# Optimization experiments

Hardware: AMD Instinct MI355X
Metric: run time of the kernel (lower is better)

The kernel has to match this reference:

```python
import jax, jax.numpy as jnp
import numpy as np

N = 100000      # entity nodes
E = 1000000     # edges per relation
D_IN = 256
HID = 128
EPS = 1e-16     # PyG softmax denominator eps
NEG_SLOPE = 0.2 # GATConv default leaky_relu slope


def _gat_conv(x, ei, Ws, Wd, a_s, a_d, b):
    """Single-head GATConv (heads=1, concat=False) with self-loops."""
    n = x.shape[0]
    loop = jnp.arange(n, dtype=ei.dtype)
    src = jnp.concatenate([ei[0], loop])  # [E+N]
    dst = jnp.concatenate([ei[1], loop])
    h_src = x @ Ws                         # [N, HID]
    h_dst = x @ Wd                         # [N, HID]
    a_src = h_src @ a_s                    # [N]
    a_dst = h_dst @ a_d                    # [N]
    e = jax.nn.leaky_relu(a_src[src] + a_dst[dst], NEG_SLOPE)  # [E+N]
    # numerically-stable softmax over incoming edges of each dst node
    m = jax.ops.segment_max(e, dst, num_segments=n)
    ex = jnp.exp(e - m[dst])
    denom = jax.ops.segment_sum(ex, dst, num_segments=n)
    alpha = ex / (denom[dst] + EPS)        # [E+N]
    out = jax.ops.segment_sum(alpha[:, None] * h_src[src], dst, num_segments=n)
    return out + b


def setup_inputs() -> dict:
    key = jax.random.key(0)
    ks = jax.random.split(key, 9)
    s_in = 1.0 / np.sqrt(D_IN)
    s_h = 1.0 / np.sqrt(HID)
    return {
        "x": jax.random.normal(ks[0], (N, D_IN), dtype=jnp.float32),
        "edge_index_r0": jax.random.randint(ks[1], (2, E), 0, N, dtype=jnp.int64)
                         if jax.config.jax_enable_x64 else jax.random.randint(ks[1], (2, E), 0, N).astype(jnp.int32),
        "edge_index_r1": jax.random.randint(ks[2], (2, E), 0, N, dtype=jnp.int64)
                         if jax.config.jax_enable_x64 else jax.random.randint(ks[2], (2, E), 0, N).astype(jnp.int32),
        "W_src": jax.random.normal(ks[3], (2, D_IN, HID), dtype=jnp.float32) * s_in,
        "W_dst": jax.random.normal(ks[4], (2, D_IN, HID), dtype=jnp.float32) * s_in,
        "att_src": jax.random.normal(ks[5], (2, HID), dtype=jnp.float32) * s_h,
        "att_dst": jax.random.normal(ks[6], (2, HID), dtype=jnp.float32) * s_h,
        "bias": jnp.zeros((2, HID), dtype=jnp.float32),
    }


def reference(x, edge_index_r0, edge_index_r1, W_src, W_dst, att_src, att_dst, bias):
    # HeteroConv aggr='sum' over the two entity->entity relations
    out = _gat_conv(x, edge_index_r0, W_src[0], W_dst[0], att_src[0], att_dst[0], bias[0])
    out = out + _gat_conv(x, edge_index_r1, W_src[1], W_dst[1], att_src[1], att_dst[1], bias[1])
    # ELU; dropout p=0.0 is identity
    return jax.nn.elu(out)
```

## Files before the change

kernel.cpp:

```cpp
#include <hip/hip_runtime.h>

typedef __attribute__((ext_vector_type(8))) __bf16 bf16x8;
typedef __attribute__((ext_vector_type(4))) float floatx4;
typedef __attribute__((ext_vector_type(2))) float floatx2;

__device__ __forceinline__ float bf2f(unsigned short u) {
    return __uint_as_float(((unsigned)u) << 16);
}
__device__ __forceinline__ unsigned short f2bf(float f) {
    unsigned u = __float_as_uint(f);
    unsigned r = u + 0x7FFFu + ((u >> 16) & 1u);
    return (unsigned short)(r >> 16);
}

__device__ __forceinline__ void canon8(const void* src, unsigned short* dst,
                                       long long idx, int f) {
    if (f) {
        *(uint4*)&dst[idx] = *(const uint4*)((const unsigned short*)src + idx);
    } else {
        const float* sf = (const float*)src;
        unsigned short v[8];
        for (int j = 0; j < 8; ++j) v[j] = f2bf(sf[idx + j]);
        *(uint4*)&dst[idx] = *(const uint4*)v;
    }
}

__global__ void detect_k(const unsigned short* __restrict__ xs, int* __restrict__ flag) {
    __shared__ int sred[256];
    int tid = threadIdx.x;
    int cnt = 0;
    for (int j = 0; j < 16; ++j) {
        unsigned short u = xs[(tid * 16 + j) * 2];
        int e = (u >> 7) & 0xFF;
        cnt += (e >= 96 && e <= 159) ? 1 : 0;
    }
    sred[tid] = cnt;
    __syncthreads();
    for (int s = 128; s > 0; s >>= 1) {
        if (tid < s) sred[tid] += sred[tid + s];
        __syncthreads();
    }
    if (tid == 0) *flag = (sred[0] > 2048) ? 1 : 0;
}

__global__ void vecb_k(const void* __restrict__ Ws, const void* __restrict__ Wd,
                       const void* __restrict__ as, const void* __restrict__ ad,
                       const void* __restrict__ b, float* __restrict__ vecs,
                       unsigned short* __restrict__ bsb, const int* __restrict__ flag) {
    int blk = blockIdx.x, tid = threadIdx.x;
    int f = *flag;
    if (blk < 2) {
        int r = blk, k = tid;
        float s = 0.f, t = 0.f;
        if (f) {
            const unsigned short* wsrow = (const unsigned short*)Ws + (size_t)r * 32768 + (size_t)k * 128;
            const unsigned short* wdrow = (const unsigned short*)Wd + (size_t)r * 32768 + (size_t)k * 128;
            const unsigned short* asr = (const unsigned short*)as + r * 128;
            const unsigned short* adr = (const unsigned short*)ad + r * 128;
            for (int h = 0; h < 128; ++h) {
                s += bf2f(wsrow[h]) * bf2f(asr[h]);
                t += bf2f(wdrow[h]) * bf2f(adr[h]);
            }
        } else {
            const float* wsrow = (const float*)Ws + (size_t)r * 32768 + (size_t)k * 128;
            const float* wdrow = (const float*)Wd + (size_t)r * 32768 + (size_t)k * 128;
            const float* asr = (const float*)as + r * 128;
            const float* adr = (const float*)ad + r * 128;
            for (int h = 0; h < 128; ++h) {
                s += wsrow[h] * asr[h];
                t += wdrow[h] * adr[h];
            }
        }
        vecs[(r * 2 + 0) * 256 + k] = s;
        vecs[(r * 2 + 1) * 256 + k] = t;
    } else {
        if (tid < 32) canon8(b, bsb, (long long)tid * 8, f);
    }
}

__global__ __launch_bounds__(256) void mix1_k(
    const int* __restrict__ ei0, const int* __restrict__ ei1,
    int* __restrict__ cnt0, int* __restrict__ cnt1,
    int* __restrict__ rank0, int* __restrict__ rank1, int E_, int histB, int period,
    const void* __restrict__ xraw, unsigned short* __restrict__ xb,
    const float* __restrict__ vecs, float* __restrict__ aout, int n, int canB,
    unsigned long long* __restrict__ pair0, unsigned long long* __restrict__ pair1,
    int ps2, int zB,
    const void* __restrict__ Ws, unsigned short* __restrict__ Bt,
    const int* __restrict__ flag) {
    __shared__ float sv[1024];
    int b = blockIdx.x, tid = threadIdx.x;
    int bq = b / period;
    if (b - bq * period == 0) {
        if (bq >= histB) return;
        int rel = bq & 1;
        int t = ((bq >> 1) << 8) + tid;
        if (t >= E_ + n) return;
        const int* ei = rel ? ei1 : ei0;
        int* cnt = rel ? cnt1 : cnt0;
        int* rank = rel ? rank1 : rank0;
        int d = (t < E_) ? ei[E_ + t] : (t - E_);
        rank[t] = atomicAdd(&cnt[d], 1);
        return;
    }
    int oid = b - bq - 1;
    if (oid < canB) {
        for (int j = 0; j < 4; ++j) sv[j * 256 + tid] = vecs[j * 256 + tid];
        __syncthreads();
        int lane = tid & 63, wave = tid >> 6;
        int row = oid * 4 + wave;
        if (row >= n) return;
        float xf[4];
        if (*flag) {
            uint2 u = *(const uint2*)((const unsigned short*)xraw + (size_t)row * 256 + lane * 4);
            xf[0] = bf2f((unsigned short)(u.x & 0xFFFF));
            xf[1] = bf2f((unsigned short)(u.x >> 16));
            xf[2] = bf2f((unsigned short)(u.y & 0xFFFF));
            xf[3] = bf2f((unsigned short)(u.y >> 16));
        } else {
            float4 f = *(const float4*)((const float*)xraw + (size_t)row * 256 + lane * 4);
            xf[0] = f.x; xf[1] = f.y; xf[2] = f.z; xf[3] = f.w;
            unsigned short v[4] = {f2bf(f.x), f2bf(f.y), f2bf(f.z), f2bf(f.w)};
            *(uint2*)&xb[(size_t)row * 256 + lane * 4] = *(const uint2*)v;
        }
        float s[4] = {0.f, 0.f, 0.f, 0.f};
        for (int j = 0; j < 4; ++j)
            for (int q = 0; q < 4; ++q)
                s[j] += xf[q] * sv[j * 256 + lane * 4 + q];
        for (int j = 0; j < 4; ++j)
            for (int off = 32; off > 0; off >>= 1)
                s[j] += __shfl_down(s[j], off);
        if (lane == 0)
            for (int j = 0; j < 4; ++j) aout[(size_t)j * n + row] = s[j];
        return;
    }
    oid -= canB;
    if (oid < 2 * zB) {
        unsigned long long* dst = (oid < zB) ? pair0 : pair1;
        int z = (oid < zB) ? oid : oid - zB;
        int idx = z * 256 + tid;
        if (idx < ps2) ((uint4*)dst)[idx] = make_uint4(0u, 0u, 0u, 0u);
        return;
    }
    oid -= 2 * zB;
    if (oid < 256) {
        int i = oid * 256 + tid;
        int f = *flag;
        int r = i >> 15, rem = i & 32767;
        int k = rem >> 7, nn = rem & 127;
        unsigned short w = f ? ((const unsigned short*)Ws)[i]
                             : f2bf(((const float*)Ws)[i]);
        Bt[(size_t)r * 32768 + nn * 256 + k] = w;
    }
}

__global__ __launch_bounds__(256) void scan_red_k(const int* __restrict__ cnt0,
                                                  const int* __restrict__ cnt1,
                                                  int* __restrict__ part,
                                                  int n, int nb) {
    __shared__ int s[256];
    int rel = blockIdx.y;
    const int* cnt = rel ? cnt1 : cnt0;
    int i = blockIdx.x * 256 + threadIdx.x;
    int v = (i < n) ? ((cnt[i] + 7) & ~7) : 0;
    s[threadIdx.x] = v;
    __syncthreads();
    for (int o = 128; o > 0; o >>= 1) {
        if (threadIdx.x < o) s[threadIdx.x] += s[threadIdx.x + o];
        __syncthreads();
    }
    if (threadIdx.x == 0) part[rel * nb + blockIdx.x] = s[0];
}

__global__ __launch_bounds__(1024) void scan_mid_k(int* __restrict__ part, int nb) {
    __shared__ int s[1024];
    int rel = blockIdx.x;
    int t = threadIdx.x;
    s[t] = (t < nb) ? part[rel * nb + t] : 0;
    __syncthreads();
    for (int o = 1; o < 1024; o <<= 1) {
        int v = (t >= o) ? s[t - o] : 0;
        __syncthreads();
        s[t] += v;
        __syncthreads();
    }
    if (t < nb) part[rel * nb + t] = (t == 0) ? 0 : s[t - 1];
}

__global__ __launch_bounds__(256) void scan_off_k(const int* __restrict__ cnt0,
                                                  const int* __restrict__ cnt1,
                                                  const int* __restrict__ part,
                                                  int* __restrict__ off0,
                                                  int* __restrict__ off1,
                                                  int n, int nb) {
    __shared__ int s[256];
    int rel = blockIdx.y;
    const int* cnt = rel ? cnt1 : cnt0;
    int* off = rel ? off1 : off0;
    int i = blockIdx.x * 256 + threadIdx.x;
    int t = threadIdx.x;
    int v = (i < n) ? ((cnt[i] + 7) & ~7) : 0;
    s[t] = v;
    __syncthreads();
    for (int o = 1; o < 256; o <<= 1) {
        int u = (t >= o) ? s[t - o] : 0;
        __syncthreads();
        s[t] += u;
        __syncthreads();
    }
    if (i < n) off[i] = part[rel * nb + blockIdx.x] + s[t] - v;
}

__global__ void fill2_k(const int* __restrict__ ei0, const int* __restrict__ ei1,
                        const float* __restrict__ avals,
                        const int* __restrict__ off0, const int* __restrict__ off1,
                        const int* __restrict__ rank0, const int* __restrict__ rank1,
                        unsigned long long* __restrict__ pair0,
                        unsigned long long* __restrict__ pair1,
                        int E_, int n) {
    int rel = blockIdx.y;
    const int* ei = rel ? ei1 : ei0;
    const float* as_ = avals + (rel ? 2 * (size_t)n : 0);
    const float* ad_ = avals + (rel ? 3 * (size_t)n : (size_t)n);
    const int* off = rel ? off1 : off0;
    const int* rank = rel ? rank1 : rank0;
    unsigned long long* pair = rel ? pair1 : pair0;
    int t = blockIdx.x * 256 + threadIdx.x;
    if (t >= E_ + n) return;
    int s, d;
    if (t < E_) { s = ei[t]; d = ei[E_ + t]; } else { s = t - E_; d = s; }
    float e = as_[s] + ad_[d];
    e = e > 0.f ? e : 0.2f * e;
    float w = __expf(e);
    int pos = off[d] + rank[t];
    pair[pos] = ((unsigned long long)__float_as_uint(w) << 32) | (unsigned)s;
}

__device__ __forceinline__ void gload_lds16(const void* g, void* l) {
    __builtin_amdgcn_global_load_lds((const __attribute__((address_space(1))) void*)g,
                                     (__attribute__((address_space(3))) void*)l, 16, 0, 0);
}

__global__ __launch_bounds__(256) void gemm_h(const void* __restrict__ x_raw,
                                              const unsigned short* __restrict__ xb,
                                              const unsigned short* __restrict__ Btg,
                                              unsigned short* __restrict__ hout, int n,
                                              const int* __restrict__ flag) {
    const unsigned short* x = (*flag) ? (const unsigned short*)x_raw : xb;
    const int r = blockIdx.y;
    const unsigned short* bt = Btg + (size_t)r * 32768;
    unsigned short* h = hout + (size_t)r * n * 128;
    const int r0 = blockIdx.x * 128;
    __shared__ __align__(16) unsigned short As[128 * 64];
    __shared__ __align__(16) unsigned short Bs[128 * 64];
    int tid = threadIdx.x;
    int lane = tid & 63, wave = tid >> 6;
    int wm = wave >> 1, wn = wave & 1;

    floatx4 acc[4][4];
    for (int mt = 0; mt < 4; ++mt)
        for (int nt = 0; nt < 4; ++nt)
            acc[mt][nt] = (floatx4){0.f, 0.f, 0.f, 0.f};

    int srow = lane >> 3;
    int q    = lane & 7;
    int m16  = lane & 15;
    int qb   = lane >> 4;

    for (int k0 = 0; k0 < 256; k0 += 64) {
        for (int i = 0; i < 4; ++i) {
            int L = wave * 4 + i;
            int row = L * 8 + srow;
            int sw = ((q ^ (row & 7)) << 3);
            int grow = min(r0 + row, n - 1);
            gload_lds16(x + (size_t)grow * 256 + k0 + sw, &As[L * 512]);
            gload_lds16(bt + (size_t)row * 256 + k0 + sw, &Bs[L * 512]);
        }
        __syncthreads();
        for (int s = 0; s < 2; ++s) {
            int qr = qb + s * 4;
            bf16x8 af[4], bfv[4];
            for (int mt = 0; mt < 4; ++mt) {
                int row = wm * 64 + mt * 16 + m16;
                af[mt] = *(const bf16x8*)&As[row * 64 + ((qr ^ (row & 7)) << 3)];
            }
            for (int nt = 0; nt < 4; ++nt) {
                int row = wn * 64 + nt * 16 + m16;
                bfv[nt] = *(const bf16x8*)&Bs[row * 64 + ((qr ^ (row & 7)) << 3)];
            }
            for (int mt = 0; mt < 4; ++mt)
                for (int nt = 0; nt < 4; ++nt)
                    acc[mt][nt] = __builtin_amdgcn_mfma_f32_16x16x32_bf16(
                        af[mt], bfv[nt], acc[mt][nt], 0, 0, 0);
        }
        __syncthreads();
    }
    for (int mt = 0; mt < 4; ++mt) {
        int baser = r0 + wm * 64 + mt * 16 + qb * 4;
        for (int nt = 0; nt < 4; ++nt) {
            int c = wn * 64 + nt * 16 + m16;
            for (int i = 0; i < 4; ++i) {
                int gr = baser + i;
                if (gr < n) h[(size_t)gr * 128 + c] = f2bf(acc[mt][nt][i]);
            }
        }
    }
}

__device__ __forceinline__ void acc8pk(floatx2* a, float w, const uint4& hv) {
    floatx2 wv = {w, w};
    const unsigned u[4] = {hv.x, hv.y, hv.z, hv.w};
#pragma unroll
    for (int k = 0; k < 4; ++k) {
        floatx2 hf;
        hf.x = __uint_as_float(u[k] << 16);
        hf.y = __uint_as_float(u[k] & 0xFFFF0000u);
        asm("v_pk_fma_f32 %0, %1, %2, %0" : "+v"(a[k]) : "v"(wv), "v"(hf));
    }
}

__device__ __forceinline__ void rel_accP(int s0, int nIt, int g, unsigned l4,
                                         const unsigned long long* __restrict__ pair,
                                         const char* __restrict__ h8,
                                         floatx2* __restrict__ a, float& den) {
    int i = s0 + g;
    unsigned long long p0 = pair[i];
    unsigned long long p1 = pair[i + 4];
    for (int it = 0; it < nIt; ++it) {
        i += 8;
        unsigned long long q0 = pair[i];
        unsigned long long q1 = pair[i + 4];
        uint4 h0 = *(const uint4*)(h8 + ((((unsigned)p0) << 8) + l4));
        uint4 h1 = *(const uint4*)(h8 + ((((unsigned)p1) << 8) + l4));
        float w0 = __uint_as_float((unsigned)(p0 >> 32));
        float w1 = __uint_as_float((unsigned)(p1 >> 32));
        den += w0 + w1;
        acc8pk(a, w0, h0);
        acc8pk(a, w1, h1);
        p0 = q0; p1 = q1;
    }
}

__global__ __launch_bounds__(256) void agg_k(
    const int* __restrict__ off0, const int* __restrict__ cnt0,
    const unsigned long long* __restrict__ pair0,
    const int* __restrict__ off1, const int* __restrict__ cnt1,
    const unsigned long long* __restrict__ pair1,
    const char* __restrict__ h0, const char* __restrict__ h1,
    const unsigned short* __restrict__ bias, void* __restrict__ out,
    int n, const int* __restrict__ flag) {
    int wave = threadIdx.x >> 6, lane = threadIdx.x & 63;
    int g = lane >> 4, l = lane & 15;
    unsigned l4 = (unsigned)l << 4;
    int d = blockIdx.x * 4 + wave;
    if (d >= n) return;

    int sA = off0[d], nItA = (cnt0[d] + 7) >> 3;
    int sB = off1[d], nItB = (cnt1[d] + 7) >> 3;

    float denA = 0.f, denB = 0.f;
    floatx2 aA[4], aB[4];
#pragma unroll
    for (int k = 0; k < 4; ++k) {
        aA[k] = (floatx2){0.f, 0.f};
        aB[k] = (floatx2){0.f, 0.f};
    }
    rel_accP(sA, nItA, g, l4, pair0, h0, aA, denA);
    rel_accP(sB, nItB, g, l4, pair1, h1, aB, denB);

    denA += __shfl_xor(denA, 16);
    denA += __shfl_xor(denA, 32);
    denB += __shfl_xor(denB, 16);
    denB += __shfl_xor(denB, 32);
    float invA = __builtin_amdgcn_rcpf(denA + 1e-16f);
    float invB = __builtin_amdgcn_rcpf(denB + 1e-16f);
    floatx2 ivA = {invA, invA}, ivB = {invB, invB};
#pragma unroll
    for (int k = 0; k < 4; ++k) {
        asm("v_pk_mul_f32 %0, %0, %1" : "+v"(aA[k]) : "v"(ivA));
        asm("v_pk_fma_f32 %0, %1, %2, %0" : "+v"(aA[k]) : "v"(aB[k]), "v"(ivB));
    }
    float t8[8] = {aA[0].x, aA[0].y, aA[1].x, aA[1].y,
                   aA[2].x, aA[2].y, aA[3].x, aA[3].y};

    uint4 b0 = *(const uint4*)&bias[l * 8];
    uint4 b1 = *(const uint4*)&bias[128 + l * 8];
    const unsigned* b0u = (const unsigned*)&b0;
    const unsigned* b1u = (const unsigned*)&b1;
    float v[8];
#pragma unroll
    for (int j = 0; j < 8; ++j) {
        float s = t8[j];
        s += __shfl_xor(s, 16);
        s += __shfl_xor(s, 32);
        unsigned w0 = b0u[j >> 1], w1 = b1u[j >> 1];
        float bb = bf2f((unsigned short)((j & 1) ? (w0 >> 16) : (w0 & 0xFFFFu)))
                 + bf2f((unsigned short)((j & 1) ? (w1 >> 16) : (w1 & 0xFFFFu)));
        float t = s + bb;
        v[j] = t > 0.f ? t : (__expf(t) - 1.f);
    }
    if (g == 0) {
        if (*flag) {
            unsigned pk[4];
            for (int j = 0; j < 4; ++j)
                pk[j] = ((unsigned)f2bf(v[2 * j + 1]) << 16) | (unsigned)f2bf(v[2 * j]);
            ((uint4*)out)[(size_t)d * 16 + l] = *(const uint4*)pk;
        } else {
            float4 f0 = make_float4(v[0], v[1], v[2], v[3]);
            float4 f1 = make_float4(v[4], v[5], v[6], v[7]);
            ((float4*)out)[(size_t)d * 32 + l * 2] = f0;
            ((float4*)out)[(size_t)d * 32 + l * 2 + 1] = f1;
        }
    }
}

static inline char* carve(char*& p, size_t bytes) {
    char* r = p;
    p += (bytes + 255) & ~(size_t)255;
    return r;
}

extern "C" void kernel_launch(void* const* d_in, const int* in_sizes, int n_in,
                              void* d_out, int out_size, void* d_ws, size_t ws_size,
                              hipStream_t stream) {
    (void)n_in; (void)out_size; (void)ws_size;
    const void* x_raw  = d_in[0];
    const int*  ei0    = (const int*)d_in[1];
    const int*  ei1    = (const int*)d_in[2];
    const void* Ws_raw = d_in[3];
    const void* Wd_raw = d_in[4];
    const void* as_raw = d_in[5];
    const void* ad_raw = d_in[6];
    const void* b_raw  = d_in[7];

    const int n = in_sizes[0] / 256;
    const int e = in_sizes[1] / 2;
    const int tot = e + n;
    const int nb = (n + 255) / 256;
    const int PS = tot + 7 * n + 32;
    const int ps2 = PS / 2;
    const int zB = (ps2 + 255) / 256;

    char* p = (char*)d_ws;
    float* avals = (float*)carve(p, (size_t)4 * n * 4);
    int*   cnt0  = (int*)carve(p, (size_t)2 * n * 4);
    int*   cnt1  = cnt0 + n;
    int*   off0  = (int*)carve(p, (size_t)n * 4);
    int*   off1  = (int*)carve(p, (size_t)n * 4);
    int*   part  = (int*)carve(p, (size_t)2 * nb * 4);
    int*   rank0 = (int*)carve(p, (size_t)tot * 4);
    int*   rank1 = (int*)carve(p, (size_t)tot * 4);
    unsigned long long* pair0 = (unsigned long long*)carve(p, (size_t)PS * 8);
    unsigned long long* pair1 = (unsigned long long*)carve(p, (size_t)PS * 8);
    float* vecs  = (float*)carve(p, 1024 * 4);
    int*   flag  = (int*)carve(p, 256);
    unsigned short* xb  = (unsigned short*)carve(p, (size_t)(n + 128) * 256 * 2);
    unsigned short* h0  = (unsigned short*)carve(p, (size_t)2 * n * 128 * 2);
    unsigned short* h1  = h0 + (size_t)n * 128;
    unsigned short* Bt  = (unsigned short*)carve(p, 65536 * 2);
    unsigned short* bsb = (unsigned short*)carve(p, 256 * 2);

    hipMemsetAsync(cnt0, 0, (size_t)2 * n * 4, stream);

    detect_k<<<1, 256, 0, stream>>>((const unsigned short*)x_raw, flag);
    vecb_k<<<3, 256, 0, stream>>>(Ws_raw, Wd_raw, as_raw, ad_raw, b_raw,
                                  vecs, bsb, flag);

    int gb = (tot + 255) / 256;
    int histB = gb * 2;
    int canB = (n + 3) / 4;
    int otherTotal = canB + 2 * zB + 256;
    int period = (otherTotal + histB - 1) / histB + 1;
    int G = histB * period;
    mix1_k<<<G, 256, 0, stream>>>(
        ei0, ei1, cnt0, cnt1, rank0, rank1, e, histB, period,
        x_raw, xb, vecs, avals, n, canB,
        pair0, pair1, ps2, zB,
        Ws_raw, Bt, flag);

    scan_red_k<<<dim3(nb, 2), 256, 0, stream>>>(cnt0, cnt1, part, n, nb);
    scan_mid_k<<<2, 1024, 0, stream>>>(part, nb);
    scan_off_k<<<dim3(nb, 2), 256, 0, stream>>>(cnt0, cnt1, part, off0, off1, n, nb);

    fill2_k<<<dim3(gb, 2), 256, 0, stream>>>(ei0, ei1, avals, off0, off1,
                                             rank0, rank1, pair0, pair1, e, n);
    gemm_h<<<dim3((n + 127) / 128, 2), 256, 0, stream>>>(x_raw, xb, Bt, h0, n, flag);

    agg_k<<<(n + 3) / 4, 256, 0, stream>>>(off0, cnt0, pair0, off1, cnt1, pair1,
                                           (const char*)h0, (const char*)h1,
                                           bsb, d_out, n, flag);
}
```

Measured before the change: 436.6 us.

## Fuse GEMM into mixed histogram kernel and pad degree counters per cache line

Moves the bf16 MFMA GEMM that produces h into the multi-role mix1 kernel, so it runs alongside the atomic degree histogram, the attention-logit computation and the pair zeroing. In the fp32 path the input is converted to bf16 on the fly instead of first writing an xb copy. The weight transpose moves into the earlier prep kernel. Degree counters are spaced 64 bytes apart to reduce atomic contention on shared lines. In exchange, mix1 gets larger LDS usage and more registers, which may lower occupancy for its lightweight block roles, and the padded counters make the memset and the scan reads larger.

```diff
diff --git a/kernel.cpp b/kernel.cpp
--- a/kernel.cpp
+++ b/kernel.cpp
@@ -43,14 +43,22 @@
     if (tid == 0) *flag = (sred[0] > 2048) ? 1 : 0;
 }
 
-__global__ void vecb_k(const void* __restrict__ Ws, const void* __restrict__ Wd,
+__global__ void prep_k(const void* __restrict__ Ws, const void* __restrict__ Wd,
                        const void* __restrict__ as, const void* __restrict__ ad,
-                       const void* __restrict__ b, float* __restrict__ vecs,
+                       const void* __restrict__ b,
+                       unsigned short* __restrict__ Bt, float* __restrict__ vecs,
                        unsigned short* __restrict__ bsb, const int* __restrict__ flag) {
     int blk = blockIdx.x, tid = threadIdx.x;
     int f = *flag;
-    if (blk < 2) {
-        int r = blk, k = tid;
+    if (blk < 256) {
+        int i = blk * 256 + tid;
+        int r = i >> 15, rem = i & 32767;
+        int k = rem >> 7, nn = rem & 127;
+        unsigned short w = f ? ((const unsigned short*)Ws)[i]
+                             : f2bf(((const float*)Ws)[i]);
+        Bt[(size_t)r * 32768 + nn * 256 + k] = w;
+    } else if (blk < 258) {
+        int r = blk - 256, k = tid;
         float s = 0.f, t = 0.f;
         if (f) {
             const unsigned short* wsrow = (const unsigned short*)Ws + (size_t)r * 32768 + (size_t)k * 128;
@@ -78,17 +86,23 @@
     }
 }
 
+__device__ __forceinline__ void gload_lds16(const void* g, void* l) {
+    __builtin_amdgcn_global_load_lds((const __attribute__((address_space(1))) void*)g,
+                                     (__attribute__((address_space(3))) void*)l, 16, 0, 0);
+}
+
 __global__ __launch_bounds__(256) void mix1_k(
     const int* __restrict__ ei0, const int* __restrict__ ei1,
-    int* __restrict__ cnt0, int* __restrict__ cnt1,
-    int* __restrict__ rank0, int* __restrict__ rank1, int E_, int histB, int period,
-    const void* __restrict__ xraw, unsigned short* __restrict__ xb,
+    int* __restrict__ cntP, int* __restrict__ rank0, int* __restrict__ rank1,
+    int E_, int histB, int period,
+    const void* __restrict__ xraw, const unsigned short* __restrict__ Btg,
+    unsigned short* __restrict__ hout, int gemmB,
     const float* __restrict__ vecs, float* __restrict__ aout, int n, int canB,
     unsigned long long* __restrict__ pair0, unsigned long long* __restrict__ pair1,
-    int ps2, int zB,
-    const void* __restrict__ Ws, unsigned short* __restrict__ Bt,
-    const int* __restrict__ flag) {
+    int ps2, int zB, const int* __restrict__ flag) {
     __shared__ float sv[1024];
+    __shared__ __align__(16) unsigned short As[128 * 64];
+    __shared__ __align__(16) unsigned short Bs[128 * 64];
     int b = blockIdx.x, tid = threadIdx.x;
     int bq = b / period;
     if (b - bq * period == 0) {
@@ -97,13 +111,86 @@
         int t = ((bq >> 1) << 8) + tid;
         if (t >= E_ + n) return;
         const int* ei = rel ? ei1 : ei0;
-        int* cnt = rel ? cnt1 : cnt0;
         int* rank = rel ? rank1 : rank0;
         int d = (t < E_) ? ei[E_ + t] : (t - E_);
-        rank[t] = atomicAdd(&cnt[d], 1);
+        rank[t] = atomicAdd(&cntP[((rel ? n : 0) + d) << 4], 1);
         return;
     }
     int oid = b - bq - 1;
+    if (oid < gemmB) {
+        int fl = *flag;
+        const int r = oid & 1;
+        const unsigned short* bt = Btg + (size_t)r * 32768;
+        unsigned short* h = hout + (size_t)r * n * 128;
+        const int r0 = (oid >> 1) * 128;
+        int lane = tid & 63, wave = tid >> 6;
+        int wm = wave >> 1, wn = wave & 1;
+        floatx4 acc[4][4];
+        for (int mt = 0; mt < 4; ++mt)
+            for (int nt = 0; nt < 4; ++nt)
+                acc[mt][nt] = (floatx4){0.f, 0.f, 0.f, 0.f};
+        int srow = lane >> 3, q = lane & 7;
+        int m16 = lane & 15, qb = lane >> 4;
+        for (int k0 = 0; k0 < 256; k0 += 64) {
+            if (fl) {
+                const unsigned short* x = (const unsigned short*)xraw;
+                for (int i = 0; i < 4; ++i) {
+                    int L = wave * 4 + i;
+                    int row = L * 8 + srow;
+                    int sw = ((q ^ (row & 7)) << 3);
+                    int grow = min(r0 + row, n - 1);
+                    gload_lds16(x + (size_t)grow * 256 + k0 + sw, &As[L * 512]);
+                    gload_lds16(bt + (size_t)row * 256 + k0 + sw, &Bs[L * 512]);
+                }
+            } else {
+                for (int i = 0; i < 4; ++i) {
+                    int L = wave * 4 + i;
+                    int row = L * 8 + srow;
+                    int sw = ((q ^ (row & 7)) << 3);
+                    gload_lds16(bt + (size_t)row * 256 + k0 + sw, &Bs[L * 512]);
+                }
+                for (int s4 = 0; s4 < 4; ++s4) {
+                    int slot = tid * 4 + s4;
+                    int row = slot >> 3, q2 = slot & 7;
+                    int grow = min(r0 + row, n - 1);
+                    const float* src = (const float*)xraw + (size_t)grow * 256 + k0 + q2 * 8;
+                    unsigned short v[8];
+                    for (int j = 0; j < 8; ++j) v[j] = f2bf(src[j]);
+                    *(uint4*)&As[row * 64 + ((q2 ^ (row & 7)) << 3)] = *(const uint4*)v;
+                }
+            }
+            __syncthreads();
+            for (int s = 0; s < 2; ++s) {
+                int qr = qb + s * 4;
+                bf16x8 af[4], bfv[4];
+                for (int mt = 0; mt < 4; ++mt) {
+                    int row = wm * 64 + mt * 16 + m16;
+                    af[mt] = *(const bf16x8*)&As[row * 64 + ((qr ^ (row & 7)) << 3)];
+                }
+                for (int nt = 0; nt < 4; ++nt) {
+                    int row = wn * 64 + nt * 16 + m16;
+                    bfv[nt] = *(const bf16x8*)&Bs[row * 64 + ((qr ^ (row & 7)) << 3)];
+                }
+                for (int mt = 0; mt < 4; ++mt)
+                    for (int nt = 0; nt < 4; ++nt)
+                        acc[mt][nt] = __builtin_amdgcn_mfma_f32_16x16x32_bf16(
+                            af[mt], bfv[nt], acc[mt][nt], 0, 0, 0);
+            }
+            __syncthreads();
+        }
+        for (int mt = 0; mt < 4; ++mt) {
+            int baser = r0 + wm * 64 + mt * 16 + qb * 4;
+            for (int nt = 0; nt < 4; ++nt) {
+                int c = wn * 64 + nt * 16 + m16;
+                for (int i = 0; i < 4; ++i) {
+                    int gr = baser + i;
+                    if (gr < n) h[(size_t)gr * 128 + c] = f2bf(acc[mt][nt][i]);
+                }
+            }
+        }
+        return;
+    }
+    oid -= gemmB;
     if (oid < canB) {
         for (int j = 0; j < 4; ++j) sv[j * 256 + tid] = vecs[j * 256 + tid];
         __syncthreads();
@@ -120,13 +207,11 @@
         } else {
             float4 f = *(const float4*)((const float*)xraw + (size_t)row * 256 + lane * 4);
             xf[0] = f.x; xf[1] = f.y; xf[2] = f.z; xf[3] = f.w;
-            unsigned short v[4] = {f2bf(f.x), f2bf(f.y), f2bf(f.z), f2bf(f.w)};
-            *(uint2*)&xb[(size_t)row * 256 + lane * 4] = *(const uint2*)v;
         }
         float s[4] = {0.f, 0.f, 0.f, 0.f};
         for (int j = 0; j < 4; ++j)
-            for (int q = 0; q < 4; ++q)
-                s[j] += xf[q] * sv[j * 256 + lane * 4 + q];
+            for (int qq = 0; qq < 4; ++qq)
+                s[j] += xf[qq] * sv[j * 256 + lane * 4 + qq];
         for (int j = 0; j < 4; ++j)
             for (int off = 32; off > 0; off >>= 1)
                 s[j] += __shfl_down(s[j], off);
@@ -140,29 +225,16 @@
         int z = (oid < zB) ? oid : oid - zB;
         int idx = z * 256 + tid;
         if (idx < ps2) ((uint4*)dst)[idx] = make_uint4(0u, 0u, 0u, 0u);
-        return;
-    }
-    oid -= 2 * zB;
-    if (oid < 256) {
-        int i = oid * 256 + tid;
-        int f = *flag;
-        int r = i >> 15, rem = i & 32767;
-        int k = rem >> 7, nn = rem & 127;
-        unsigned short w = f ? ((const unsigned short*)Ws)[i]
-                             : f2bf(((const float*)Ws)[i]);
-        Bt[(size_t)r * 32768 + nn * 256 + k] = w;
-    }
-}
-
-__global__ __launch_bounds__(256) void scan_red_k(const int* __restrict__ cnt0,
-                                                  const int* __restrict__ cnt1,
+    }
+}
+
+__global__ __launch_bounds__(256) void scan_red_k(const int* __restrict__ cntP,
                                                   int* __restrict__ part,
                                                   int n, int nb) {
     __shared__ int s[256];
     int rel = blockIdx.y;
-    const int* cnt = rel ? cnt1 : cnt0;
     int i = blockIdx.x * 256 + threadIdx.x;
-    int v = (i < n) ? ((cnt[i] + 7) & ~7) : 0;
+    int v = (i < n) ? ((cntP[((rel ? n : 0) + i) << 4] + 7) & ~7) : 0;
     s[threadIdx.x] = v;
     __syncthreads();
     for (int o = 128; o > 0; o >>= 1) {
@@ -187,19 +259,17 @@
     if (t < nb) part[rel * nb + t] = (t == 0) ? 0 : s[t - 1];
 }
 
-__global__ __launch_bounds__(256) void scan_off_k(const int* __restrict__ cnt0,
-                                                  const int* __restrict__ cnt1,
+__global__ __launch_bounds__(256) void scan_off_k(const int* __restrict__ cntP,
                                                   const int* __restrict__ part,
                                                   int* __restrict__ off0,
                                                   int* __restrict__ off1,
                                                   int n, int nb) {
     __shared__ int s[256];
     int rel = blockIdx.y;
-    const int* cnt = rel ? cnt1 : cnt0;
     int* off = rel ? off1 : off0;
     int i = blockIdx.x * 256 + threadIdx.x;
     int t = threadIdx.x;
-    int v = (i < n) ? ((cnt[i] + 7) & ~7) : 0;
+    int v = (i < n) ? ((cntP[((rel ? n : 0) + i) << 4] + 7) & ~7) : 0;
     s[t] = v;
     __syncthreads();
     for (int o = 1; o < 256; o <<= 1) {
@@ -236,77 +306,6 @@
     pair[pos] = ((unsigned long long)__float_as_uint(w) << 32) | (unsigned)s;
 }
 
-__device__ __forceinline__ void gload_lds16(const void* g, void* l) {
-    __builtin_amdgcn_global_load_lds((const __attribute__((address_space(1))) void*)g,
-                                     (__attribute__((address_space(3))) void*)l, 16, 0, 0);
-}
-
-__global__ __launch_bounds__(256) void gemm_h(const void* __restrict__ x_raw,
-                                              const unsigned short* __restrict__ xb,
-                                              const unsigned short* __restrict__ Btg,
-                                              unsigned short* __restrict__ hout, int n,
-                                              const int* __restrict__ flag) {
-    const unsigned short* x = (*flag) ? (const unsigned short*)x_raw : xb;
-    const int r = blockIdx.y;
-    const unsigned short* bt = Btg + (size_t)r * 32768;
-    unsigned short* h = hout + (size_t)r * n * 128;
-    const int r0 = blockIdx.x * 128;
-    __shared__ __align__(16) unsigned short As[128 * 64];
-    __shared__ __align__(16) unsigned short Bs[128 * 64];
-    int tid = threadIdx.x;
-    int lane = tid & 63, wave = tid >> 6;
-    int wm = wave >> 1, wn = wave & 1;
-
-    floatx4 acc[4][4];
-    for (int mt = 0; mt < 4; ++mt)
-        for (int nt = 0; nt < 4; ++nt)
-            acc[mt][nt] = (floatx4){0.f, 0.f, 0.f, 0.f};
-
-    int srow = lane >> 3;
-    int q    = lane & 7;
-    int m16  = lane & 15;
-    int qb   = lane >> 4;
-
-    for (int k0 = 0; k0 < 256; k0 += 64) {
-        for (int i = 0; i < 4; ++i) {
-            int L = wave * 4 + i;
-            int row = L * 8 + srow;
-            int sw = ((q ^ (row & 7)) << 3);
-            int grow = min(r0 + row, n - 1);
-            gload_lds16(x + (size_t)grow * 256 + k0 + sw, &As[L * 512]);
-            gload_lds16(bt + (size_t)row * 256 + k0 + sw, &Bs[L * 512]);
-        }
-        __syncthreads();
-        for (int s = 0; s < 2; ++s) {
-            int qr = qb + s * 4;
-            bf16x8 af[4], bfv[4];
-            for (int mt = 0; mt < 4; ++mt) {
-                int row = wm * 64 + mt * 16 + m16;
-                af[mt] = *(const bf16x8*)&As[row * 64 + ((qr ^ (row & 7)) << 3)];
-            }
-            for (int nt = 0; nt < 4; ++nt) {
-                int row = wn * 64 + nt * 16 + m16;
-                bfv[nt] = *(const bf16x8*)&Bs[row * 64 + ((qr ^ (row & 7)) << 3)];
-            }
-            for (int mt = 0; mt < 4; ++mt)
-                for (int nt = 0; nt < 4; ++nt)
-                    acc[mt][nt] = __builtin_amdgcn_mfma_f32_16x16x32_bf16(
-                        af[mt], bfv[nt], acc[mt][nt], 0, 0, 0);
-        }
-        __syncthreads();
-    }
-    for (int mt = 0; mt < 4; ++mt) {
-        int baser = r0 + wm * 64 + mt * 16 + qb * 4;
-        for (int nt = 0; nt < 4; ++nt) {
-            int c = wn * 64 + nt * 16 + m16;
-            for (int i = 0; i < 4; ++i) {
-                int gr = baser + i;
-                if (gr < n) h[(size_t)gr * 128 + c] = f2bf(acc[mt][nt][i]);
-            }
-        }
-    }
-}
-
 __device__ __forceinline__ void acc8pk(floatx2* a, float w, const uint4& hv) {
     floatx2 wv = {w, w};
     const unsigned u[4] = {hv.x, hv.y, hv.z, hv.w};
@@ -342,9 +341,9 @@
 }
 
 __global__ __launch_bounds__(256) void agg_k(
-    const int* __restrict__ off0, const int* __restrict__ cnt0,
+    const int* __restrict__ off0, const int* __restrict__ off1,
+    const int* __restrict__ cntP,
     const unsigned long long* __restrict__ pair0,
-    const int* __restrict__ off1, const int* __restrict__ cnt1,
     const unsigned long long* __restrict__ pair1,
     const char* __restrict__ h0, const char* __restrict__ h1,
     const unsigned short* __restrict__ bias, void* __restrict__ out,
@@ -355,8 +354,8 @@
     int d = blockIdx.x * 4 + wave;
     if (d >= n) return;
 
-    int sA = off0[d], nItA = (cnt0[d] + 7) >> 3;
-    int sB = off1[d], nItB = (cnt1[d] + 7) >> 3;
+    int sA = off0[d], nItA = (cntP[d << 4] + 7) >> 3;
+    int sB = off1[d], nItB = (cntP[(n + d) << 4] + 7) >> 3;
 
     float denA = 0.f, denB = 0.f;
     floatx2 aA[4], aB[4];
@@ -443,8 +442,7 @@
 
     char* p = (char*)d_ws;
     float* avals = (float*)carve(p, (size_t)4 * n * 4);
-    int*   cnt0  = (int*)carve(p, (size_t)2 * n * 4);
-    int*   cnt1  = cnt0 + n;
+    int*   cntP  = (int*)carve(p, (size_t)2 * n * 64);
     int*   off0  = (int*)carve(p, (size_t)n * 4);
     int*   off1  = (int*)carve(p, (size_t)n * 4);
     int*   part  = (int*)carve(p, (size_t)2 * nb * 4);
@@ -454,39 +452,38 @@
     unsigned long long* pair1 = (unsigned long long*)carve(p, (size_t)PS * 8);
     float* vecs  = (float*)carve(p, 1024 * 4);
     int*   flag  = (int*)carve(p, 256);
-    unsigned short* xb  = (unsigned short*)carve(p, (size_t)(n + 128) * 256 * 2);
     unsigned short* h0  = (unsigned short*)carve(p, (size_t)2 * n * 128 * 2);
     unsigned short* h1  = h0 + (size_t)n * 128;
     unsigned short* Bt  = (unsigned short*)carve(p, 65536 * 2);
     unsigned short* bsb = (unsigned short*)carve(p, 256 * 2);
 
-    hipMemsetAsync(cnt0, 0, (size_t)2 * n * 4, stream);
+    hipMemsetAsync(cntP, 0, (size_t)2 * n * 64, stream);
 
     detect_k<<<1, 256, 0, stream>>>((const unsigned short*)x_raw, flag);
-    vecb_k<<<3, 256, 0, stream>>>(Ws_raw, Wd_raw, as_raw, ad_raw, b_raw,
-                                  vecs, bsb, flag);
+    prep_k<<<259, 256, 0, stream>>>(Ws_raw, Wd_raw, as_raw, ad_raw, b_raw,
+                                    Bt, vecs, bsb, flag);
 
     int gb = (tot + 255) / 256;
     int histB = gb * 2;
+    int gemmB = ((n + 127) / 128) * 2;
     int canB = (n + 3) / 4;
-    int otherTotal = canB + 2 * zB + 256;
+    int otherTotal = gemmB + canB + 2 * zB;
     int period = (otherTotal + histB - 1) / histB + 1;
     int G = histB * period;
     mix1_k<<<G, 256, 0, stream>>>(
-        ei0, ei1, cnt0, cnt1, rank0, rank1, e, histB, period,
-        x_raw, xb, vecs, avals, n, canB,
-        pair0, pair1, ps2, zB,
-        Ws_raw, Bt, flag);
-
-    scan_red_k<<<dim3(nb, 2), 256, 0, stream>>>(cnt0, cnt1, part, n, nb);
+        ei0, ei1, cntP, rank0, rank1, e, histB, period,
+        x_raw, Bt, h0, gemmB,
+        vecs, avals, n, canB,
+        pair0, pair1, ps2, zB, flag);
+
+    scan_red_k<<<dim3(nb, 2), 256, 0, stream>>>(cntP, part, n, nb);
     scan_mid_k<<<2, 1024, 0, stream>>>(part, nb);
-    scan_off_k<<<dim3(nb, 2), 256, 0, stream>>>(cnt0, cnt1, part, off0, off1, n, nb);
+    scan_off_k<<<dim3(nb, 2), 256, 0, stream>>>(cntP, part, off0, off1, n, nb);
 
     fill2_k<<<dim3(gb, 2), 256, 0, stream>>>(ei0, ei1, avals, off0, off1,
                                              rank0, rank1, pair0, pair1, e, n);
-    gemm_h<<<dim3((n + 127) / 128, 2), 256, 0, stream>>>(x_raw, xb, Bt, h0, n, flag);
-
-    agg_k<<<(n + 3) / 4, 256, 0, stream>>>(off0, cnt0, pair0, off1, cnt1, pair1,
+
+    agg_k<<<(n + 3) / 4, 256, 0, stream>>>(off0, off1, cntP, pair0, pair1,
                                            (const char*)h0, (const char*)h1,
                                            bsb, d_out, n, flag);
 }
```

New measurement: 503.7 us. 1.15x slower.
